# Performance work log

Measured on AMD Instinct MI355X. Metric: run time of the kernel, lower is better.

The kernel has to match this reference:

```python
import jax, jax.numpy as jnp
import numpy as np

C = 3  # RGB channels

# Scharr kernels, depthwise: shape [C_out, C_in/groups, kh, kw] = [C, 1, 3, 3]
_KX = np.array([[-3., 0., 3.], [-10., 0., 10.], [-3., 0., 3.]], dtype=np.float32)
_KY = np.array([[-3., -10., -3.], [0., 0., 0.], [3., 10., 3.]], dtype=np.float32)
KERNEL_X = jnp.tile(jnp.asarray(_KX)[None, None], (C, 1, 1, 1))
KERNEL_Y = jnp.tile(jnp.asarray(_KY)[None, None], (C, 1, 1, 1))


def _depthwise3x3(img, kernel):
    # img: [B, C, H, W]; kernel: [C, 1, 3, 3]; groups=C, stride 1, padding 1
    return jax.lax.conv_general_dilated(
        img, kernel,
        window_strides=(1, 1),
        padding=((1, 1), (1, 1)),
        dimension_numbers=('NCHW', 'OIHW', 'NCHW'),
        feature_group_count=C)


def _scharr_grad(img):
    gx = _depthwise3x3(img, KERNEL_X)
    gy = _depthwise3x3(img, KERNEL_Y)
    return jnp.abs(gx) + jnp.abs(gy)


def setup_inputs() -> dict:
    key = jax.random.key(0)
    kx, kg = jax.random.split(key)
    x = jax.random.uniform(kx, (16, 3, 512, 512), dtype=jnp.float32)
    gt = jax.random.uniform(kg, (16, 3, 512, 512), dtype=jnp.float32)
    return {"x": x, "gt": gt}


def reference(x, gt):
    loss = jnp.abs(_scharr_grad(x) - _scharr_grad(gt))
    return jnp.mean(loss)  # size_average=True
```

## Files before the change

kernel.cpp:

```cpp
#include <hip/hip_runtime.h>

#define Wd 512
#define Hd 512
#define NIMG 48
#define ROWS 8
#define STRIPS (NIMG * (Hd / ROWS))
#define NBLOCKS (STRIPS / 4)
constexpr float INV_N = 1.0f / (float)((long long)NIMG * Hd * Wd);

__device__ __forceinline__ float scharr_pix(const float r0[10], const float r1[10],
                                            const float r2[10], int j) {
    float tl = r0[j], tm = r0[j + 1], tr = r0[j + 2];
    float ml = r1[j],                  mr = r1[j + 2];
    float bl = r2[j], bm = r2[j + 1], br = r2[j + 2];
    float gx = 3.f * (tr - tl) + 10.f * (mr - ml) + 3.f * (br - bl);
    float gy = 3.f * (bl - tl) + 10.f * (bm - tm) + 3.f * (br - tr);
    return fabsf(gx) + fabsf(gy);
}

__device__ __forceinline__ void load_row(const float* __restrict__ img, int h,
                                         int c0, int lane, float r[10]) {
    if ((unsigned)h < (unsigned)Hd) {
        const float* p = img + (size_t)h * Wd + c0;
        float4 b0 = *reinterpret_cast<const float4*>(p);
        float4 b1 = *reinterpret_cast<const float4*>(p + 4);
        r[1] = b0.x; r[2] = b0.y; r[3] = b0.z; r[4] = b0.w;
        r[5] = b1.x; r[6] = b1.y; r[7] = b1.z; r[8] = b1.w;
        float lv = __shfl_up(b1.w, 1, 64);
        float rv = __shfl_down(b0.x, 1, 64);
        r[0] = (lane > 0)  ? lv : 0.f;
        r[9] = (lane < 63) ? rv : 0.f;
    } else {
        #pragma unroll
        for (int k = 0; k < 10; ++k) r[k] = 0.f;
    }
}

__global__ void __launch_bounds__(256)
scharr_loss_kernel(const float* __restrict__ x, const float* __restrict__ gt,
                   float* __restrict__ partials) {
    int wid   = threadIdx.x >> 6;
    int lane  = threadIdx.x & 63;
    int strip = blockIdx.x * 4 + wid;
    int img   = strip >> 6;
    int h0    = (strip & 63) * ROWS;
    int c0    = lane * 8;

    const float* __restrict__ xb = x  + (size_t)img * Hd * Wd;
    const float* __restrict__ gb = gt + (size_t)img * Hd * Wd;

    float rx[3][10], rg[3][10];
    load_row(xb, h0 - 1, c0, lane, rx[0]);
    load_row(xb, h0,     c0, lane, rx[1]);
    load_row(gb, h0 - 1, c0, lane, rg[0]);
    load_row(gb, h0,     c0, lane, rg[1]);

    float sum = 0.f;
    #pragma unroll
    for (int i = 0; i < ROWS; ++i) {
        const int c0i = i % 3, c1i = (i + 1) % 3, c2i = (i + 2) % 3;
        load_row(xb, h0 + i + 1, c0, lane, rx[c2i]);
        load_row(gb, h0 + i + 1, c0, lane, rg[c2i]);
        #pragma unroll
        for (int j = 0; j < 8; ++j) {
            float a = scharr_pix(rx[c0i], rx[c1i], rx[c2i], j);
            float b = scharr_pix(rg[c0i], rg[c1i], rg[c2i], j);
            sum += fabsf(a - b);
        }
    }

    #pragma unroll
    for (int off = 32; off > 0; off >>= 1)
        sum += __shfl_down(sum, off, 64);

    __shared__ float ws[4];
    if (lane == 0) ws[wid] = sum;
    __syncthreads();
    if (threadIdx.x == 0)
        partials[blockIdx.x] = ws[0] + ws[1] + ws[2] + ws[3];
}

__global__ void __launch_bounds__(256)
reduce_partials_kernel(const float* __restrict__ partials, float* __restrict__ out) {
    float s = 0.f;
    #pragma unroll
    for (int k = 0; k < NBLOCKS / 256; ++k)
        s += partials[k * 256 + threadIdx.x];
    #pragma unroll
    for (int off = 32; off > 0; off >>= 1)
        s += __shfl_down(s, off, 64);
    __shared__ float ws[4];
    int lane = threadIdx.x & 63;
    int wid  = threadIdx.x >> 6;
    if (lane == 0) ws[wid] = s;
    __syncthreads();
    if (threadIdx.x == 0)
        out[0] = (ws[0] + ws[1] + ws[2] + ws[3]) * INV_N;
}

extern "C" void kernel_launch(void* const* d_in, const int* in_sizes, int n_in,
                              void* d_out, int out_size, void* d_ws, size_t ws_size,
                              hipStream_t stream) {
    const float* x  = (const float*)d_in[0];
    const float* gt = (const float*)d_in[1];
    float* out      = (float*)d_out;
    float* partials = (float*)d_ws;

    scharr_loss_kernel<<<NBLOCKS, 256, 0, stream>>>(x, gt, partials);
    reduce_partials_kernel<<<1, 256, 0, stream>>>(partials, out);
}
```

Measured before the change: 29.59 us.

## Stage 16-row tiles in LDS via direct global-to-LDS loads with block swizzle

Each block now loads an 18-row halo tile for both x and gt straight into shared memory using the global_load_lds builtin, then each wave computes 4 rows from LDS. Before, every wave streamed its own 8-row strip from global memory and reloaded the halo rows. The change cuts halo overfetch, moves loads to the asynchronous LDS path, and swizzles block order across images. In exchange it uses about 72KB of LDS per block, which limits occupancy, and there is no overlap between the load and compute phases inside a block.

```diff
diff --git a/kernel.cpp b/kernel.cpp
--- a/kernel.cpp
+++ b/kernel.cpp
@@ -3,10 +3,16 @@
 #define Wd 512
 #define Hd 512
 #define NIMG 48
-#define ROWS 8
-#define STRIPS (NIMG * (Hd / ROWS))
-#define NBLOCKS (STRIPS / 4)
+#define RB 16
+#define LR (RB + 2)
+#define NBLK (NIMG * (Hd / RB))
 constexpr float INV_N = 1.0f / (float)((long long)NIMG * Hd * Wd);
+
+__device__ __forceinline__ void gload_lds16(const float* g, float* l) {
+    __builtin_amdgcn_global_load_lds(
+        (const __attribute__((address_space(1))) void*)g,
+        (__attribute__((address_space(3))) void*)l, 16, 0, 0);
+}
 
 __device__ __forceinline__ float scharr_pix(const float r0[10], const float r1[10],
                                             const float r2[10], int j) {
@@ -18,62 +24,75 @@
     return fabsf(gx) + fabsf(gy);
 }
 
-__device__ __forceinline__ void load_row(const float* __restrict__ img, int h,
-                                         int c0, int lane, float r[10]) {
-    if ((unsigned)h < (unsigned)Hd) {
-        const float* p = img + (size_t)h * Wd + c0;
-        float4 b0 = *reinterpret_cast<const float4*>(p);
-        float4 b1 = *reinterpret_cast<const float4*>(p + 4);
-        r[1] = b0.x; r[2] = b0.y; r[3] = b0.z; r[4] = b0.w;
-        r[5] = b1.x; r[6] = b1.y; r[7] = b1.z; r[8] = b1.w;
-        float lv = __shfl_up(b1.w, 1, 64);
-        float rv = __shfl_down(b0.x, 1, 64);
-        r[0] = (lane > 0)  ? lv : 0.f;
-        r[9] = (lane < 63) ? rv : 0.f;
-    } else {
-        #pragma unroll
-        for (int k = 0; k < 10; ++k) r[k] = 0.f;
-    }
+__device__ __forceinline__ void lds_row(const float* __restrict__ row, int lane,
+                                        float r[10]) {
+    float4 b0 = *reinterpret_cast<const float4*>(row + lane * 8);
+    float4 b1 = *reinterpret_cast<const float4*>(row + lane * 8 + 4);
+    r[1] = b0.x; r[2] = b0.y; r[3] = b0.z; r[4] = b0.w;
+    r[5] = b1.x; r[6] = b1.y; r[7] = b1.z; r[8] = b1.w;
+    float lv = __shfl_up(b1.w, 1, 64);
+    float rv = __shfl_down(b0.x, 1, 64);
+    r[0] = (lane > 0)  ? lv : 0.f;
+    r[9] = (lane < 63) ? rv : 0.f;
 }
 
 __global__ void __launch_bounds__(256)
 scharr_loss_kernel(const float* __restrict__ x, const float* __restrict__ gt,
                    float* __restrict__ partials) {
-    int wid   = threadIdx.x >> 6;
-    int lane  = threadIdx.x & 63;
-    int strip = blockIdx.x * 4 + wid;
-    int img   = strip >> 6;
-    int h0    = (strip & 63) * ROWS;
-    int c0    = lane * 8;
+    __shared__ float lb[2][LR][Wd];
+    __shared__ float ws[4];
+
+    int wid  = threadIdx.x >> 6;
+    int lane = threadIdx.x & 63;
+
+    int b   = blockIdx.x;
+    int swz = (b & 7) * (NBLK / 8) + (b >> 3);
+    int img = swz >> 5;
+    int h0  = (swz & 31) * RB;
 
     const float* __restrict__ xb = x  + (size_t)img * Hd * Wd;
     const float* __restrict__ gb = gt + (size_t)img * Hd * Wd;
 
+    int is   = wid >> 1;
+    int half = wid & 1;
+    const float* __restrict__ sb = is ? gb : xb;
+    #pragma unroll
+    for (int t = 0; t < LR; ++t) {
+        int gh = h0 - 1 + t;
+        float* dst = &lb[is][t][half * 256];
+        if ((unsigned)gh < (unsigned)Hd) {
+            gload_lds16(sb + (size_t)gh * Wd + half * 256 + lane * 4, dst);
+        } else {
+            *reinterpret_cast<float4*>(dst + lane * 4) =
+                make_float4(0.f, 0.f, 0.f, 0.f);
+        }
+    }
+    __syncthreads();
+
+    int r0 = wid * 4;
     float rx[3][10], rg[3][10];
-    load_row(xb, h0 - 1, c0, lane, rx[0]);
-    load_row(xb, h0,     c0, lane, rx[1]);
-    load_row(gb, h0 - 1, c0, lane, rg[0]);
-    load_row(gb, h0,     c0, lane, rg[1]);
+    lds_row(&lb[0][r0][0],     lane, rx[0]);
+    lds_row(&lb[0][r0 + 1][0], lane, rx[1]);
+    lds_row(&lb[1][r0][0],     lane, rg[0]);
+    lds_row(&lb[1][r0 + 1][0], lane, rg[1]);
 
     float sum = 0.f;
     #pragma unroll
-    for (int i = 0; i < ROWS; ++i) {
-        const int c0i = i % 3, c1i = (i + 1) % 3, c2i = (i + 2) % 3;
-        load_row(xb, h0 + i + 1, c0, lane, rx[c2i]);
-        load_row(gb, h0 + i + 1, c0, lane, rg[c2i]);
+    for (int i = 0; i < 4; ++i) {
+        const int c0 = i % 3, c1 = (i + 1) % 3, c2 = (i + 2) % 3;
+        lds_row(&lb[0][r0 + i + 2][0], lane, rx[c2]);
+        lds_row(&lb[1][r0 + i + 2][0], lane, rg[c2]);
         #pragma unroll
         for (int j = 0; j < 8; ++j) {
-            float a = scharr_pix(rx[c0i], rx[c1i], rx[c2i], j);
-            float b = scharr_pix(rg[c0i], rg[c1i], rg[c2i], j);
-            sum += fabsf(a - b);
+            float a = scharr_pix(rx[c0], rx[c1], rx[c2], j);
+            float g = scharr_pix(rg[c0], rg[c1], rg[c2], j);
+            sum += fabsf(a - g);
         }
     }
 
     #pragma unroll
     for (int off = 32; off > 0; off >>= 1)
         sum += __shfl_down(sum, off, 64);
-
-    __shared__ float ws[4];
     if (lane == 0) ws[wid] = sum;
     __syncthreads();
     if (threadIdx.x == 0)
@@ -84,7 +103,7 @@
 reduce_partials_kernel(const float* __restrict__ partials, float* __restrict__ out) {
     float s = 0.f;
     #pragma unroll
-    for (int k = 0; k < NBLOCKS / 256; ++k)
+    for (int k = 0; k < NBLK / 256; ++k)
         s += partials[k * 256 + threadIdx.x];
     #pragma unroll
     for (int off = 32; off > 0; off >>= 1)
@@ -106,6 +125,6 @@
     float* out      = (float*)d_out;
     float* partials = (float*)d_ws;
 
-    scharr_loss_kernel<<<NBLOCKS, 256, 0, stream>>>(x, gt, partials);
+    scharr_loss_kernel<<<NBLK, 256, 0, stream>>>(x, gt, partials);
     reduce_partials_kernel<<<1, 256, 0, stream>>>(partials, out);
 }
```

New measurement: 24.98 us. 1.18x faster.
